# Kernel optimization log

Measured on AMD Instinct MI355X. Metric: run time of the kernel, lower is better.

## Reference

```python
import jax, jax.numpy as jnp
import numpy as np
import math

B, S, D, H, L = 2, 2048, 2048, 16, 512
HD = D // H          # head dim = 128
DIM_KV = 256         # scale = sqrt(DIM_KV // 2) = sqrt(128)
EPS = 1e-5


def _layer_norm(x, g, b):
    m = jnp.mean(x, axis=-1, keepdims=True)
    v = jnp.var(x, axis=-1, keepdims=True)
    return (x - m) * jax.lax.rsqrt(v + EPS) * g + b


def setup_inputs() -> dict:
    key = jax.random.key(0)
    ks = jax.random.split(key, 10)
    s = 0.02
    return {
        "x": jax.random.normal(ks[0], (B, S, D), dtype=jnp.float32),
        "mask": jnp.zeros((B, S), dtype=bool),  # True = padded position
        "wq_down": jax.random.normal(ks[1], (D, L), dtype=jnp.float32) * s,
        "bq_down": jnp.zeros((L,), dtype=jnp.float32),
        "gq_ln": jnp.ones((L,), dtype=jnp.float32),
        "bq_ln": jnp.zeros((L,), dtype=jnp.float32),
        "wq_up": jax.random.normal(ks[2], (L, D), dtype=jnp.float32) * s,
        "bq_up": jnp.zeros((D,), dtype=jnp.float32),
        "wkv_down": jax.random.normal(ks[3], (D, L), dtype=jnp.float32) * s,
        "bkv_down": jnp.zeros((L,), dtype=jnp.float32),
        "gkv_ln": jnp.ones((L,), dtype=jnp.float32),
        "bkv_ln": jnp.zeros((L,), dtype=jnp.float32),
        "wkv_up": jax.random.normal(ks[4], (L, 2 * D), dtype=jnp.float32) * s,
        "bkv_up": jnp.zeros((2 * D,), dtype=jnp.float32),
        "w_out": jax.random.normal(ks[5], (D, D), dtype=jnp.float32) * s,
        "b_out": jnp.zeros((D,), dtype=jnp.float32),
    }


def reference(x, mask, wq_down, bq_down, gq_ln, bq_ln, wq_up, bq_up,
              wkv_down, bkv_down, gkv_ln, bkv_ln, wkv_up, bkv_up, w_out, b_out):
    # low-rank query path: down-proj -> LN -> up-proj
    q_lat = _layer_norm(x @ wq_down + bq_down, gq_ln, bq_ln)      # [B,S,L]
    q = q_lat @ wq_up + bq_up                                      # [B,S,D]
    # low-rank KV path (compressed_kv is the MLA latent / cache entry)
    kv_lat = _layer_norm(x @ wkv_down + bkv_down, gkv_ln, bkv_ln)  # [B,S,L]
    kv = kv_lat @ wkv_up + bkv_up                                  # [B,S,2D]
    k, v = jnp.split(kv, 2, axis=-1)                               # [B,S,D] each

    def heads(t):
        return t.reshape(B, S, H, HD).transpose(0, 2, 1, 3)        # [B,H,S,HD]

    qh, kh, vh = heads(q), heads(k), heads(v)
    scale = 1.0 / math.sqrt(DIM_KV // 2)
    scores = jnp.einsum('bhqd,bhkd->bhqk', qh, kh) * scale          # [B,H,S,S]
    neg_inf = jnp.finfo(scores.dtype).min
    # padding mask (True = masked) broadcast over heads and queries
    scores = jnp.where(mask[:, None, None, :], neg_inf, scores)
    causal = jnp.triu(jnp.ones((S, S), dtype=bool), k=1)
    scores = jnp.where(causal, neg_inf, scores)
    attn = jax.nn.softmax(scores, axis=-1)
    out = jnp.einsum('bhqk,bhkd->bhqd', attn, vh)                   # [B,H,S,HD]
    out = out.transpose(0, 2, 1, 3).reshape(B, S, D)
    return out @ w_out + b_out
```

## Files before the change

kernel.cpp:

```cpp
#include <hip/hip_runtime.h>
#include <math.h>
#include <type_traits>

typedef unsigned short u16;
typedef __attribute__((ext_vector_type(8))) short bf16x8;
typedef __attribute__((ext_vector_type(4))) float f32x4;

#define B_  2
#define S_  2048
#define D_  2048
#define H_  16
#define HD_ 128
#define L_  512
constexpr float EPS   = 1e-5f;
constexpr float SCALE = 0.08838834764831845f;

__device__ __forceinline__ u16 f2bf(float x) {
    unsigned u = __float_as_uint(x);
    u += 0x7fffu + ((u >> 16) & 1u);
    return (u16)(u >> 16);
}
__device__ __forceinline__ float bf2f(u16 v) {
    return __uint_as_float(((unsigned)v) << 16);
}

__device__ __forceinline__ void gl_lds16(const u16* g, u16* l) {
    __builtin_amdgcn_global_load_lds(
        (const __attribute__((address_space(1))) unsigned int*)g,
        (__attribute__((address_space(3))) unsigned int*)l, 16, 0, 0);
}

template <typename OutT, int BN>
__global__ __launch_bounds__(256)
void gemm_mfma_kernel(const u16* __restrict__ A, const u16* __restrict__ Bt,
                      const float* __restrict__ biasA,
                      const float* __restrict__ biasB, OutT* __restrict__ C,
                      int M, int N, int K, int lda, int nsplit) {
    constexpr int NJ = BN / 32;
    __shared__ __align__(16) u16 As[128 * 32];
    __shared__ __align__(16) u16 Bs[BN * 32];

    const int tid  = threadIdx.x;
    const int wave = tid >> 6, lane = tid & 63;
    const int l15  = lane & 15, g = lane >> 4;
    const int wm   = wave >> 1, wn = wave & 1;
    const int m0   = blockIdx.y * 128, n0 = blockIdx.x * BN;

    const int sr = lane >> 2;
    const int sc = lane & 3;
    const int swz = (l15 >> 1) & 3;

    f32x4 acc[4][NJ];
#pragma unroll
    for (int i = 0; i < 4; ++i)
#pragma unroll
        for (int j = 0; j < NJ; ++j) acc[i][j] = (f32x4)0.f;

    for (int k0 = 0; k0 < K; k0 += 32) {
#pragma unroll
        for (int t = 0; t < 2; ++t) {
            const int r  = wave * 32 + t * 16 + sr;
            const int c  = sc ^ ((r >> 1) & 3);
            gl_lds16(A + (size_t)(m0 + r) * lda + k0 + c * 8,
                     &As[(wave * 32 + t * 16) * 32]);
        }
#pragma unroll
        for (int t = 0; t < BN / 64; ++t) {
            const int r  = wave * (BN / 4) + t * 16 + sr;
            const int c  = sc ^ ((r >> 1) & 3);
            gl_lds16(Bt + (size_t)(n0 + r) * K + k0 + c * 8,
                     &Bs[(wave * (BN / 4) + t * 16) * 32]);
        }
        __syncthreads();

        bf16x8 af[4], bfr[NJ];
#pragma unroll
        for (int i = 0; i < 4; ++i) {
            const int ra = wm * 64 + i * 16 + l15;
            af[i]  = *(const bf16x8*)&As[ra * 32 + (g ^ swz) * 8];
        }
#pragma unroll
        for (int j = 0; j < NJ; ++j) {
            const int rb = wn * (BN / 2) + j * 16 + l15;
            bfr[j] = *(const bf16x8*)&Bs[rb * 32 + (g ^ swz) * 8];
        }
#pragma unroll
        for (int i = 0; i < 4; ++i)
#pragma unroll
            for (int j = 0; j < NJ; ++j)
                acc[i][j] = __builtin_amdgcn_mfma_f32_16x16x32_bf16(
                    af[i], bfr[j], acc[i][j], 0, 0, 0);
        __syncthreads();
    }

#pragma unroll
    for (int j = 0; j < NJ; ++j) {
        const int n  = n0 + wn * (BN / 2) + j * 16 + l15;
        const float bv = (n < nsplit) ? biasA[n] : biasB[n - nsplit];
#pragma unroll
        for (int i = 0; i < 4; ++i) {
            const int mb = m0 + wm * 64 + i * 16 + g * 4;
#pragma unroll
            for (int r = 0; r < 4; ++r) {
                float v = acc[i][j][r] + bv;
                if constexpr (std::is_same_v<OutT, float>)
                    C[(size_t)(mb + r) * N + n] = v;
                else
                    C[(size_t)(mb + r) * N + n] = f2bf(v);
            }
        }
    }
}

__global__ __launch_bounds__(256)
void cast_bf16_kernel(const float* __restrict__ src, u16* __restrict__ dst,
                      int n4) {
    const int i = blockIdx.x * 256 + threadIdx.x;
    if (i < n4) {
        float4 f = ((const float4*)src)[i];
        ushort4 o;
        o.x = f2bf(f.x); o.y = f2bf(f.y); o.z = f2bf(f.z); o.w = f2bf(f.w);
        ((ushort4*)dst)[i] = o;
    }
}

__global__ __launch_bounds__(256)
void batched_transpose_kernel(const float* __restrict__ wqd,
                              const float* __restrict__ wkvd,
                              const float* __restrict__ wqu,
                              const float* __restrict__ wkvu,
                              const float* __restrict__ wo,
                              u16* __restrict__ wd_t,
                              u16* __restrict__ wqu_t,
                              u16* __restrict__ wkvu_t,
                              u16* __restrict__ wout_t) {
    int bid = blockIdx.x;
    const float* W; u16* Wt; int K, N;
    if (bid < 256)       { W = wqd;  Wt = wd_t;                      K = 2048; N = 512; }
    else if (bid < 512)  { W = wkvd; Wt = wd_t + (size_t)512 * 2048; K = 2048; N = 512;  bid -= 256; }
    else if (bid < 768)  { W = wqu;  Wt = wqu_t;                     K = 512;  N = 2048; bid -= 512; }
    else if (bid < 1280) { W = wkvu; Wt = wkvu_t;                    K = 512;  N = 4096; bid -= 768; }
    else                 { W = wo;   Wt = wout_t;                    K = 2048; N = 2048; bid -= 1280; }
    const int nblk = N / 64;
    const int n0 = (bid % nblk) * 64, k0 = (bid / nblk) * 64;

    __shared__ u16 T[64][72];
    const int t = threadIdx.x;
    {
        const int kr = t >> 2, nc = (t & 3) * 16;
#pragma unroll
        for (int v = 0; v < 4; ++v) {
            float4 f = *(const float4*)&W[(size_t)(k0 + kr) * N + n0 + nc + v * 4];
            T[nc + v * 4 + 0][kr] = f2bf(f.x);
            T[nc + v * 4 + 1][kr] = f2bf(f.y);
            T[nc + v * 4 + 2][kr] = f2bf(f.z);
            T[nc + v * 4 + 3][kr] = f2bf(f.w);
        }
    }
    __syncthreads();
    {
        const int nr = t >> 2, kc = (t & 3) * 16;
        union { u16 u[16]; uint4 q[2]; } o;
#pragma unroll
        for (int i = 0; i < 16; ++i) o.u[i] = T[nr][kc + i];
        uint4* dst = (uint4*)&Wt[(size_t)(n0 + nr) * K + k0 + kc];
        dst[0] = o.q[0]; dst[1] = o.q[1];
    }
}

__global__ __launch_bounds__(256)
void layernorm_fused_kernel(u16* __restrict__ buf,
                            const float* __restrict__ gq,
                            const float* __restrict__ bq,
                            const float* __restrict__ gkv,
                            const float* __restrict__ bkv) {
    const int r    = blockIdx.x;
    const int half = r & 1;
    u16* p = buf + (size_t)(r >> 1) * 1024 + half * 512;
    const float* g    = half ? gkv : gq;
    const float* bvec = half ? bkv : bq;
    const int tid = threadIdx.x;

    float x0 = bf2f(p[tid]), x1 = bf2f(p[tid + 256]);
    float s  = x0 + x1;
    float sq = x0 * x0 + x1 * x1;

    __shared__ float red[8];
    __shared__ float stats[2];

#pragma unroll
    for (int off = 32; off; off >>= 1) {
        s  += __shfl_down(s, off);
        sq += __shfl_down(sq, off);
    }
    const int wave = tid >> 6;
    if ((tid & 63) == 0) { red[wave] = s; red[wave + 4] = sq; }
    __syncthreads();
    if (tid == 0) {
        float ts = red[0] + red[1] + red[2] + red[3];
        float tq = red[4] + red[5] + red[6] + red[7];
        float mean = ts / (float)L_;
        float var  = tq / (float)L_ - mean * mean;
        stats[0] = mean;
        stats[1] = rsqrtf(var + EPS);
    }
    __syncthreads();
    const float mean = stats[0], rstd = stats[1];
    p[tid]       = f2bf((x0 - mean) * rstd * g[tid]       + bvec[tid]);
    p[tid + 256] = f2bf((x1 - mean) * rstd * g[tid + 256] + bvec[tid + 256]);
}

__global__ __launch_bounds__(256)
void vtrans_kernel(const u16* __restrict__ kvbf, u16* __restrict__ vt) {
    const int s0 = blockIdx.x * 64;
    const int h  = blockIdx.y, b = blockIdx.z;
    __shared__ u16 T[64][136];
    const int t = threadIdx.x;
    {
        const int sl = t >> 2, dc = (t & 3) * 32;
        const uint4* src = (const uint4*)(kvbf +
            ((size_t)(b * S_ + s0 + sl) * (2 * D_) + D_ + h * HD_ + dc));
        uint4 a0 = src[0], a1 = src[1], a2 = src[2], a3 = src[3];
        *(uint4*)&T[sl][dc]      = a0;
        *(uint4*)&T[sl][dc + 8]  = a1;
        *(uint4*)&T[sl][dc + 16] = a2;
        *(uint4*)&T[sl][dc + 24] = a3;
    }
    __syncthreads();
    {
        const int d = t >> 1, sh = (t & 1) * 32;
        union { u16 u[32]; uint4 q[4]; } buf;
#pragma unroll
        for (int i = 0; i < 32; ++i) buf.u[i] = T[sh + i][d];
        uint4* dst = (uint4*)(vt +
            ((size_t)((b * H_ + h) * HD_ + d)) * S_ + s0 + sh);
        dst[0] = buf.q[0]; dst[1] = buf.q[1];
        dst[2] = buf.q[2]; dst[3] = buf.q[3];
    }
}

#define PPITCH 72

__global__ __launch_bounds__(256)
void flash_attn_kernel(const u16* __restrict__ qbf, const u16* __restrict__ kvbf,
                       const u16* __restrict__ vt,
                       const unsigned char* __restrict__ mask,
                       u16* __restrict__ out) {
    const int x    = blockIdx.x;
    const int qgrp = (S_ / 64 - 1) - (x >> 5);
    const int hb   = x & 31;
    const int h    = hb >> 1, b = hb & 1;
    const int tid  = threadIdx.x;
    const int wave = tid >> 6, lane = tid & 63;
    const int l15  = lane & 15, g = lane >> 4;
    const int q0   = qgrp * 64 + wave * 16;

    __shared__ __align__(16) u16 Ks[2][64][128];
    __shared__ __align__(16) u16 Vs[2][128][64];
    __shared__ __align__(16) u16 Pl[4][16][PPITCH];

    const u16* kbase = kvbf + (size_t)b * S_ * (2 * D_) + h * HD_;
    const u16* vbase = vt + (size_t)((b * H_ + h) * HD_) * S_;
    const unsigned char* mbase = mask + b * S_;

    const int kr_l = lane >> 4;
    const int kb_l = (lane & 15) * 16;
    const int vr_l = lane >> 3;
    const int vb_l = (lane & 7) * 16;

    auto STAGE = [&](int bi, int k0s) {
#pragma unroll
        for (int j = 0; j < 4; ++j) {
            const int rr = wave * 16 + j * 4 + kr_l;
            gl_lds16(kbase + (size_t)(k0s + rr) * (2 * D_) +
                         ((kb_l ^ ((rr & 7) << 4)) >> 1),
                     &Ks[bi][wave * 16 + j * 4][0]);
            const int rv = wave * 32 + j * 8 + vr_l;
            gl_lds16(vbase + (size_t)rv * S_ + k0s +
                         ((vb_l ^ ((rv & 7) << 4)) >> 1),
                     &Vs[bi][wave * 32 + j * 8][0]);
        }
    };

    bf16x8 qf[4];
#pragma unroll
    for (int c = 0; c < 4; ++c)
        qf[c] = *(const bf16x8*)(qbf +
            (size_t)(b * S_ + q0 + l15) * D_ + h * HD_ + c * 32 + g * 8);

    bf16x8 ones;
#pragma unroll
    for (int j = 0; j < 8; ++j) ones[j] = (short)0x3f80;

    f32x4 o[8];
#pragma unroll
    for (int i = 0; i < 8; ++i) o[i] = (f32x4)0.f;
    f32x4 osum = (f32x4)0.f;
    float m_run[4];
#pragma unroll
    for (int r = 0; r < 4; ++r) m_run[r] = -INFINITY;

    const int qb  = q0 + 4 * g;
    const int ksw = (l15 & 7) << 4;
    const int nt  = qgrp + 1;

    STAGE(0, 0);
    __syncthreads();

    for (int kt = 0; kt < nt; ++kt) {
        const int k0  = kt * 64;
        const int cur = kt & 1;
        if (kt + 1 < nt) STAGE(cur ^ 1, k0 + 64);

        float nb[4];
#pragma unroll
        for (int cc = 0; cc < 4; ++cc)
            nb[cc] = mbase[k0 + cc * 16 + l15] ? -INFINITY : 0.f;

        f32x4 s[4];
#pragma unroll
        for (int cc = 0; cc < 4; ++cc) {
            bf16x8 kf[4];
#pragma unroll
            for (int c = 0; c < 4; ++c)
                kf[c] = *(const bf16x8*)&Ks[cur][cc * 16 + l15]
                    [((c * 64 + g * 16) ^ ksw) >> 1];
            f32x4 t = (f32x4)0.f;
#pragma unroll
            for (int c = 0; c < 4; ++c)
                t = __builtin_amdgcn_mfma_f32_16x16x32_bf16(qf[c], kf[c], t, 0, 0, 0);
            s[cc] = t;
        }

#pragma unroll
        for (int cc = 0; cc < 4; ++cc)
#pragma unroll
            for (int r = 0; r < 4; ++r)
                s[cc][r] = fmaf(s[cc][r], SCALE, nb[cc]);

        if (kt == nt - 1) {
#pragma unroll
            for (int cc = 0; cc < 4; ++cc) {
                const int kk = k0 + cc * 16 + l15;
#pragma unroll
                for (int r = 0; r < 4; ++r)
                    if (kk > qb + r) s[cc][r] = -INFINITY;
            }
        }

        float tm[4];
#pragma unroll
        for (int r = 0; r < 4; ++r)
            tm[r] = fmaxf(fmaxf(s[0][r], s[1][r]), fmaxf(s[2][r], s[3][r]));
#pragma unroll
        for (int off = 1; off < 16; off <<= 1)
#pragma unroll
            for (int r = 0; r < 4; ++r)
                tm[r] = fmaxf(tm[r], __shfl_xor(tm[r], off));

        bool chg = false;
#pragma unroll
        for (int r = 0; r < 4; ++r) chg |= (tm[r] > m_run[r] + 8.f);
        if (__any(chg)) {
            f32x4 av;
#pragma unroll
            for (int r = 0; r < 4; ++r) {
                const float nm = fmaxf(m_run[r], tm[r]);
                av[r] = __expf(m_run[r] - nm);
                m_run[r] = nm;
            }
#pragma unroll
            for (int i = 0; i < 8; ++i) o[i] *= av;
            osum *= av;
        }

#pragma unroll
        for (int cc = 0; cc < 4; ++cc)
#pragma unroll
            for (int r = 0; r < 4; ++r)
                Pl[wave][4 * g + r][cc * 16 + l15] =
                    f2bf(__expf(s[cc][r] - m_run[r]));

        const bf16x8 pf0 = *(const bf16x8*)&Pl[wave][l15][g * 8];
        const bf16x8 pf1 = *(const bf16x8*)&Pl[wave][l15][32 + g * 8];

#pragma unroll
        for (int i = 0; i < 8; ++i) {
            bf16x8 vf0 = *(const bf16x8*)&Vs[cur][16 * i + l15]
                [((g * 16) ^ ksw) >> 1];
            bf16x8 vf1 = *(const bf16x8*)&Vs[cur][16 * i + l15]
                [((g * 16 + 64) ^ ksw) >> 1];
            o[i] = __builtin_amdgcn_mfma_f32_16x16x32_bf16(pf0, vf0, o[i], 0, 0, 0);
            o[i] = __builtin_amdgcn_mfma_f32_16x16x32_bf16(pf1, vf1, o[i], 0, 0, 0);
        }
        osum = __builtin_amdgcn_mfma_f32_16x16x32_bf16(pf0, ones, osum, 0, 0, 0);
        osum = __builtin_amdgcn_mfma_f32_16x16x32_bf16(pf1, ones, osum, 0, 0, 0);

        __syncthreads();
    }

    float inv[4];
#pragma unroll
    for (int r = 0; r < 4; ++r) inv[r] = 1.0f / osum[r];
#pragma unroll
    for (int i = 0; i < 8; ++i)
#pragma unroll
        for (int r = 0; r < 4; ++r)
            out[(size_t)(b * S_ + q0 + 4 * g + r) * D_ +
                h * HD_ + 16 * i + l15] = f2bf(o[i][r] * inv[r]);
}

extern "C" void kernel_launch(void* const* d_in, const int* in_sizes, int n_in,
                              void* d_out, int out_size, void* d_ws, size_t ws_size,
                              hipStream_t stream) {
    const float* x        = (const float*)d_in[0];
    const unsigned char* mask = (const unsigned char*)d_in[1];
    const float* wq_down  = (const float*)d_in[2];
    const float* bq_down  = (const float*)d_in[3];
    const float* gq_ln    = (const float*)d_in[4];
    const float* bq_ln    = (const float*)d_in[5];
    const float* wq_up    = (const float*)d_in[6];
    const float* bq_up    = (const float*)d_in[7];
    const float* wkv_down = (const float*)d_in[8];
    const float* bkv_down = (const float*)d_in[9];
    const float* gkv_ln   = (const float*)d_in[10];
    const float* bkv_ln   = (const float*)d_in[11];
    const float* wkv_up   = (const float*)d_in[12];
    const float* bkv_up   = (const float*)d_in[13];
    const float* w_out    = (const float*)d_in[14];
    const float* b_out    = (const float*)d_in[15];
    float* out = (float*)d_out;

    char* ws = (char*)d_ws;
    u16* x_bf    = (u16*)(ws);
    u16* vt      = (u16*)(ws);
    u16* lat     = (u16*)(ws + (16u << 20));
    u16* attn_bf = (u16*)(ws + (16u << 20));
    u16* wd_t    = (u16*)(ws + (24u << 20));
    u16* wkvu_t  = (u16*)(ws + (28u << 20));
    u16* wqu_t   = (u16*)(ws + (32u << 20));
    u16* wout_t  = (u16*)(ws + (34u << 20));
    u16* q_bf    = (u16*)(ws + (42u << 20));
    u16* kv_bf   = (u16*)(ws + (58u << 20));

    const int M = B_ * S_;
    dim3 blk(256);

    cast_bf16_kernel<<<(M * D_ / 4 + 255) / 256, blk, 0, stream>>>(x, x_bf, M * D_ / 4);
    batched_transpose_kernel<<<2304, blk, 0, stream>>>(
        wq_down, wkv_down, wq_up, wkv_up, w_out, wd_t, wqu_t, wkvu_t, wout_t);

    gemm_mfma_kernel<u16, 64><<<dim3((2 * L_) / 64, M / 128), blk, 0, stream>>>(
        x_bf, wd_t, bq_down, bkv_down, lat, M, 2 * L_, D_, D_, L_);

    layernorm_fused_kernel<<<2 * M, blk, 0, stream>>>(lat, gq_ln, bq_ln, gkv_ln, bkv_ln);

    gemm_mfma_kernel<u16, 128><<<dim3(2 * D_ / 128, M / 128), blk, 0, stream>>>(
        lat + L_, wkvu_t, bkv_up, bkv_up, kv_bf, M, 2 * D_, L_, 2 * L_, 2 * D_);
    gemm_mfma_kernel<u16, 128><<<dim3(D_ / 128, M / 128), blk, 0, stream>>>(
        lat, wqu_t, bq_up, bq_up, q_bf, M, D_, L_, 2 * L_, D_);

    vtrans_kernel<<<dim3(S_ / 64, H_, B_), blk, 0, stream>>>(kv_bf, vt);

    flash_attn_kernel<<<dim3((S_ / 64) * H_ * B_), blk, 0, stream>>>(
        q_bf, kv_bf, vt, mask, attn_bf);

    gemm_mfma_kernel<float, 128><<<dim3(D_ / 128, M / 128), blk, 0, stream>>>(
        attn_bf, wout_t, b_out, b_out, out, M, D_, D_, D_, D_);
}
```

Baseline: 369.2 us.

## Fuse V transpose into KV-up GEMM epilogue and merge prep kernels

The KV up-projection GEMM now writes K into its own buffer and writes V directly in the head-major transposed layout. This removes the separate vtrans kernel and the extra read and write of V. The input cast and the weight transposes are merged into a single prep launch, and s_setprio is raised around the MFMA sections of the attention kernel. The fused V store uses narrow strided 8-byte writes, which may coalesce less well than the old transpose kernel.

```diff
diff --git a/kernel.cpp b/kernel.cpp
--- a/kernel.cpp
+++ b/kernel.cpp
@@ -30,12 +30,13 @@
         (__attribute__((address_space(3))) unsigned int*)l, 16, 0, 0);
 }
 
-template <typename OutT, int BN>
+template <typename OutT, int BN, bool VFUSE = false>
 __global__ __launch_bounds__(256)
 void gemm_mfma_kernel(const u16* __restrict__ A, const u16* __restrict__ Bt,
                       const float* __restrict__ biasA,
                       const float* __restrict__ biasB, OutT* __restrict__ C,
-                      int M, int N, int K, int lda, int nsplit) {
+                      u16* __restrict__ VT,
+                      int M, int N, int K, int lda, int ldc, int nsplit) {
     constexpr int NJ = BN / 32;
     __shared__ __align__(16) u16 As[128 * 32];
     __shared__ __align__(16) u16 Bs[BN * 32];
@@ -97,44 +98,55 @@
     for (int j = 0; j < NJ; ++j) {
         const int n  = n0 + wn * (BN / 2) + j * 16 + l15;
         const float bv = (n < nsplit) ? biasA[n] : biasB[n - nsplit];
-#pragma unroll
-        for (int i = 0; i < 4; ++i) {
-            const int mb = m0 + wm * 64 + i * 16 + g * 4;
-#pragma unroll
-            for (int r = 0; r < 4; ++r) {
-                float v = acc[i][j][r] + bv;
-                if constexpr (std::is_same_v<OutT, float>)
-                    C[(size_t)(mb + r) * N + n] = v;
-                else
-                    C[(size_t)(mb + r) * N + n] = f2bf(v);
+        bool vstore = false;
+        if constexpr (VFUSE) vstore = (n0 >= D_);
+        if (vstore) {
+            const int dg = n - D_;
+            const int hh = dg >> 7, dd = dg & 127;
+            u16* vrow = VT + ((size_t)(((m0 >> 11) * H_ + hh) * HD_ + dd)) * S_;
+#pragma unroll
+            for (int i = 0; i < 4; ++i) {
+                const int mb = m0 + wm * 64 + i * 16 + g * 4;
+                ushort4 o;
+                o.x = f2bf(acc[i][j][0] + bv);
+                o.y = f2bf(acc[i][j][1] + bv);
+                o.z = f2bf(acc[i][j][2] + bv);
+                o.w = f2bf(acc[i][j][3] + bv);
+                *(ushort4*)&vrow[mb & (S_ - 1)] = o;
             }
+        } else {
+#pragma unroll
+            for (int i = 0; i < 4; ++i) {
+                const int mb = m0 + wm * 64 + i * 16 + g * 4;
+#pragma unroll
+                for (int r = 0; r < 4; ++r) {
+                    float v = acc[i][j][r] + bv;
+                    if constexpr (std::is_same_v<OutT, float>)
+                        C[(size_t)(mb + r) * ldc + n] = v;
+                    else
+                        C[(size_t)(mb + r) * ldc + n] = f2bf(v);
+                }
+            }
         }
     }
 }
 
 __global__ __launch_bounds__(256)
-void cast_bf16_kernel(const float* __restrict__ src, u16* __restrict__ dst,
-                      int n4) {
-    const int i = blockIdx.x * 256 + threadIdx.x;
-    if (i < n4) {
-        float4 f = ((const float4*)src)[i];
+void prep_kernel(const float* __restrict__ wqd,  const float* __restrict__ wkvd,
+                 const float* __restrict__ wqu,  const float* __restrict__ wkvu,
+                 const float* __restrict__ wo,   const float* __restrict__ x,
+                 u16* __restrict__ wd_t,  u16* __restrict__ wqu_t,
+                 u16* __restrict__ wkvu_t, u16* __restrict__ wout_t,
+                 u16* __restrict__ x_bf) {
+    int bid = blockIdx.x;
+    if (bid >= 2304) {
+        const int i = (bid - 2304) * 256 + threadIdx.x;
+        float4 f = ((const float4*)x)[i];
         ushort4 o;
         o.x = f2bf(f.x); o.y = f2bf(f.y); o.z = f2bf(f.z); o.w = f2bf(f.w);
-        ((ushort4*)dst)[i] = o;
-    }
-}
-
-__global__ __launch_bounds__(256)
-void batched_transpose_kernel(const float* __restrict__ wqd,
-                              const float* __restrict__ wkvd,
-                              const float* __restrict__ wqu,
-                              const float* __restrict__ wkvu,
-                              const float* __restrict__ wo,
-                              u16* __restrict__ wd_t,
-                              u16* __restrict__ wqu_t,
-                              u16* __restrict__ wkvu_t,
-                              u16* __restrict__ wout_t) {
-    int bid = blockIdx.x;
+        ((ushort4*)x_bf)[i] = o;
+        return;
+    }
     const float* W; u16* Wt; int K, N;
     if (bid < 256)       { W = wqd;  Wt = wd_t;                      K = 2048; N = 512; }
     else if (bid < 512)  { W = wkvd; Wt = wd_t + (size_t)512 * 2048; K = 2048; N = 512;  bid -= 256; }
@@ -210,39 +222,10 @@
     p[tid + 256] = f2bf((x1 - mean) * rstd * g[tid + 256] + bvec[tid + 256]);
 }
 
+#define PPITCH 72
+
 __global__ __launch_bounds__(256)
-void vtrans_kernel(const u16* __restrict__ kvbf, u16* __restrict__ vt) {
-    const int s0 = blockIdx.x * 64;
-    const int h  = blockIdx.y, b = blockIdx.z;
-    __shared__ u16 T[64][136];
-    const int t = threadIdx.x;
-    {
-        const int sl = t >> 2, dc = (t & 3) * 32;
-        const uint4* src = (const uint4*)(kvbf +
-            ((size_t)(b * S_ + s0 + sl) * (2 * D_) + D_ + h * HD_ + dc));
-        uint4 a0 = src[0], a1 = src[1], a2 = src[2], a3 = src[3];
-        *(uint4*)&T[sl][dc]      = a0;
-        *(uint4*)&T[sl][dc + 8]  = a1;
-        *(uint4*)&T[sl][dc + 16] = a2;
-        *(uint4*)&T[sl][dc + 24] = a3;
-    }
-    __syncthreads();
-    {
-        const int d = t >> 1, sh = (t & 1) * 32;
-        union { u16 u[32]; uint4 q[4]; } buf;
-#pragma unroll
-        for (int i = 0; i < 32; ++i) buf.u[i] = T[sh + i][d];
-        uint4* dst = (uint4*)(vt +
-            ((size_t)((b * H_ + h) * HD_ + d)) * S_ + s0 + sh);
-        dst[0] = buf.q[0]; dst[1] = buf.q[1];
-        dst[2] = buf.q[2]; dst[3] = buf.q[3];
-    }
-}
-
-#define PPITCH 72
-
-__global__ __launch_bounds__(256)
-void flash_attn_kernel(const u16* __restrict__ qbf, const u16* __restrict__ kvbf,
+void flash_attn_kernel(const u16* __restrict__ qbf, const u16* __restrict__ kbf,
                        const u16* __restrict__ vt,
                        const unsigned char* __restrict__ mask,
                        u16* __restrict__ out) {
@@ -259,7 +242,7 @@
     __shared__ __align__(16) u16 Vs[2][128][64];
     __shared__ __align__(16) u16 Pl[4][16][PPITCH];
 
-    const u16* kbase = kvbf + (size_t)b * S_ * (2 * D_) + h * HD_;
+    const u16* kbase = kbf + (size_t)b * S_ * D_ + h * HD_;
     const u16* vbase = vt + (size_t)((b * H_ + h) * HD_) * S_;
     const unsigned char* mbase = mask + b * S_;
 
@@ -272,7 +255,7 @@
 #pragma unroll
         for (int j = 0; j < 4; ++j) {
             const int rr = wave * 16 + j * 4 + kr_l;
-            gl_lds16(kbase + (size_t)(k0s + rr) * (2 * D_) +
+            gl_lds16(kbase + (size_t)(k0s + rr) * D_ +
                          ((kb_l ^ ((rr & 7) << 4)) >> 1),
                      &Ks[bi][wave * 16 + j * 4][0]);
             const int rv = wave * 32 + j * 8 + vr_l;
@@ -318,6 +301,7 @@
             nb[cc] = mbase[k0 + cc * 16 + l15] ? -INFINITY : 0.f;
 
         f32x4 s[4];
+        __builtin_amdgcn_s_setprio(1);
 #pragma unroll
         for (int cc = 0; cc < 4; ++cc) {
             bf16x8 kf[4];
@@ -331,6 +315,7 @@
                 t = __builtin_amdgcn_mfma_f32_16x16x32_bf16(qf[c], kf[c], t, 0, 0, 0);
             s[cc] = t;
         }
+        __builtin_amdgcn_s_setprio(0);
 
 #pragma unroll
         for (int cc = 0; cc < 4; ++cc)
@@ -384,6 +369,7 @@
         const bf16x8 pf0 = *(const bf16x8*)&Pl[wave][l15][g * 8];
         const bf16x8 pf1 = *(const bf16x8*)&Pl[wave][l15][32 + g * 8];
 
+        __builtin_amdgcn_s_setprio(1);
 #pragma unroll
         for (int i = 0; i < 8; ++i) {
             bf16x8 vf0 = *(const bf16x8*)&Vs[cur][16 * i + l15]
@@ -395,6 +381,7 @@
         }
         osum = __builtin_amdgcn_mfma_f32_16x16x32_bf16(pf0, ones, osum, 0, 0, 0);
         osum = __builtin_amdgcn_mfma_f32_16x16x32_bf16(pf1, ones, osum, 0, 0, 0);
+        __builtin_amdgcn_s_setprio(0);
 
         __syncthreads();
     }
@@ -441,30 +428,33 @@
     u16* wqu_t   = (u16*)(ws + (32u << 20));
     u16* wout_t  = (u16*)(ws + (34u << 20));
     u16* q_bf    = (u16*)(ws + (42u << 20));
-    u16* kv_bf   = (u16*)(ws + (58u << 20));
+    u16* k_bf    = (u16*)(ws + (58u << 20));
 
     const int M = B_ * S_;
     dim3 blk(256);
 
-    cast_bf16_kernel<<<(M * D_ / 4 + 255) / 256, blk, 0, stream>>>(x, x_bf, M * D_ / 4);
-    batched_transpose_kernel<<<2304, blk, 0, stream>>>(
-        wq_down, wkv_down, wq_up, wkv_up, w_out, wd_t, wqu_t, wkvu_t, wout_t);
+    prep_kernel<<<10496, blk, 0, stream>>>(
+        wq_down, wkv_down, wq_up, wkv_up, w_out, x,
+        wd_t, wqu_t, wkvu_t, wout_t, x_bf);
 
     gemm_mfma_kernel<u16, 64><<<dim3((2 * L_) / 64, M / 128), blk, 0, stream>>>(
-        x_bf, wd_t, bq_down, bkv_down, lat, M, 2 * L_, D_, D_, L_);
+        x_bf, wd_t, bq_down, bkv_down, lat, nullptr,
+        M, 2 * L_, D_, D_, 2 * L_, L_);
 
     layernorm_fused_kernel<<<2 * M, blk, 0, stream>>>(lat, gq_ln, bq_ln, gkv_ln, bkv_ln);
 
-    gemm_mfma_kernel<u16, 128><<<dim3(2 * D_ / 128, M / 128), blk, 0, stream>>>(
-        lat + L_, wkvu_t, bkv_up, bkv_up, kv_bf, M, 2 * D_, L_, 2 * L_, 2 * D_);
+    gemm_mfma_kernel<u16, 128, true><<<dim3(2 * D_ / 128, M / 128), blk, 0, stream>>>(
+        lat + L_, wkvu_t, bkv_up, bkv_up, k_bf, vt,
+        M, 2 * D_, L_, 2 * L_, D_, 2 * D_);
+
     gemm_mfma_kernel<u16, 128><<<dim3(D_ / 128, M / 128), blk, 0, stream>>>(
-        lat, wqu_t, bq_up, bq_up, q_bf, M, D_, L_, 2 * L_, D_);
-
-    vtrans_kernel<<<dim3(S_ / 64, H_, B_), blk, 0, stream>>>(kv_bf, vt);
+        lat, wqu_t, bq_up, bq_up, q_bf, nullptr,
+        M, D_, L_, 2 * L_, D_, D_);
 
     flash_attn_kernel<<<dim3((S_ / 64) * H_ * B_), blk, 0, stream>>>(
-        q_bf, kv_bf, vt, mask, attn_bf);
+        q_bf, k_bf, vt, mask, attn_bf);
 
     gemm_mfma_kernel<float, 128><<<dim3(D_ / 128, M / 128), blk, 0, stream>>>(
-        attn_bf, wout_t, b_out, b_out, out, M, D_, D_, D_, D_);
-}
+        attn_bf, wout_t, b_out, b_out, out, nullptr,
+        M, D_, D_, D_, D_, D_);
+}
```

Result: faster. 357.3 us (-3.2%).
